# Kernel tuning notes

Measured on AMD Instinct MI355X. Metric: run time of the kernel, lower is better.

Reference implementation:

```python
import jax, jax.numpy as jnp
import numpy as np

B, N, NID, V, GH, PHI, RHO = 8, 256, 64, 128, 128, 256, 128
BN = B * N
EPS = 1e-5


def _layernorm(x, g, b):
    m = jnp.mean(x, axis=-1, keepdims=True)
    v = jnp.var(x, axis=-1, keepdims=True)
    return (x - m) * jax.lax.rsqrt(v + EPS) * g + b


def _edges(A):
    # dense adjacency -> flat batched edge list, exactly as mask.nonzero() ordering
    bidx = jnp.arange(B)[:, None, None]
    ii = jnp.arange(N)[None, :, None]
    jj = jnp.arange(N)[None, None, :]
    src = jnp.broadcast_to(bidx * N + ii, (B, N, N)).reshape(-1)  # edge_index[0] = b*N+i
    tgt = jnp.broadcast_to(bidx * N + jj, (B, N, N)).reshape(-1)  # edge_index[1] = b*N+j
    w = A.reshape(-1)
    valid = w != 0
    rel = (w > 0).astype(jnp.int32)
    return src, tgt, w, valid, rel


def _rgcn(H, src, tgt, valid, rel, Wrel, Wroot, bias):
    # torch_geometric RGCNConv: mean aggregation per relation at target + root + bias
    x_src = H[src]  # (E, d) gather
    out = H @ Wroot + bias
    for r in range(2):
        m = (valid & (rel == r)).astype(H.dtype)  # (E,)
        s = jax.ops.segment_sum(x_src * m[:, None], tgt, num_segments=BN)
        c = jax.ops.segment_sum(m, tgt, num_segments=BN)
        out = out + (s / jnp.maximum(c, 1.0)[:, None]) @ Wrel[r]
    return out


def setup_inputs() -> dict:
    key = jax.random.key(0)
    ks = jax.random.split(key, 24)
    p = lambda k, shape: jax.random.normal(k, shape, dtype=jnp.float32) * 0.02
    z = lambda *shape: jnp.zeros(shape, jnp.float32)
    return {
        "A": jax.random.normal(ks[0], (B, N, N), dtype=jnp.float32),
        "X": jax.random.normal(ks[1], (B, N, NID), dtype=jnp.float32),
        "home_mask": (jax.random.uniform(ks[2], (B, N)) > 0.5).astype(jnp.float32),
        "emb1_w": p(ks[3], (NID, V)), "emb1_b": z(V),
        "emb2_w": p(ks[4], (V, V)), "emb2_b": z(V),
        "rgcn_w_0": p(ks[5], (2, V, GH)), "rgcn_root_0": p(ks[6], (V, GH)), "rgcn_bias_0": z(GH),
        "lina_w_0": p(ks[7], (GH, GH)), "lina_b_0": z(GH),
        "linb_w_0": p(ks[8], (GH, GH)), "linb_b_0": z(GH),
        "rgcn_w_1": p(ks[9], (2, GH, GH)), "rgcn_root_1": p(ks[10], (GH, GH)), "rgcn_bias_1": z(GH),
        "lina_w_1": p(ks[11], (GH, GH)), "lina_b_1": z(GH),
        "linb_w_1": p(ks[12], (GH, GH)), "linb_b_1": z(GH),
        "norm_g": jnp.ones((GH,), jnp.float32), "norm_b": z(GH),
        "phi_w1": p(ks[13], (GH, PHI)), "phi_b1": z(PHI),
        "phi_w2": p(ks[14], (PHI, PHI)), "phi_b2": z(PHI),
        "rho_w1": p(ks[15], (PHI, RHO)), "rho_b1": z(RHO),
        "rho_w2": p(ks[16], (RHO, 1)), "rho_b2": z(1),
    }


def reference(A, X, home_mask, emb1_w, emb1_b, emb2_w, emb2_b,
              rgcn_w_0, rgcn_root_0, rgcn_bias_0, lina_w_0, lina_b_0, linb_w_0, linb_b_0,
              rgcn_w_1, rgcn_root_1, rgcn_bias_1, lina_w_1, lina_b_1, linb_w_1, linb_b_1,
              norm_g, norm_b, phi_w1, phi_b1, phi_w2, phi_b2,
              rho_w1, rho_b1, rho_w2, rho_b2):
    away_mask = 1.0 - home_mask
    H = jax.nn.relu(X @ emb1_w + emb1_b)
    H = (H @ emb2_w + emb2_b).reshape(BN, V)

    src, tgt, w, valid, rel = _edges(A)
    aw = jnp.abs(w) * valid.astype(w.dtype)  # |edge_weight|, zero for masked-out edges

    blocks = [
        (rgcn_w_0, rgcn_root_0, rgcn_bias_0, lina_w_0, lina_b_0, linb_w_0, linb_b_0),
        (rgcn_w_1, rgcn_root_1, rgcn_bias_1, lina_w_1, lina_b_1, linb_w_1, linb_b_1),
    ]
    agg = jnp.zeros_like(H)
    for (Wrel, Wroot, bias, law, lab, lbw, lbb) in blocks:
        H = H + agg
        H2 = _rgcn(H, src, tgt, valid, rel, Wrel, Wroot, bias)
        # gather-scale-scatter: agg[src] += H2[tgt] * |w|
        agg = jax.ops.segment_sum(H2[tgt] * aw[:, None], src, num_segments=BN)
        agg = jax.nn.relu(_layernorm(agg, norm_g, norm_b))  # dropout = identity (eval)
        agg = jax.nn.relu(agg @ law + lab)
        agg = agg @ lbw + lbb
    H = (H + agg).reshape(B, N, GH)

    # DeepSet phi (dropout = identity)
    h = jax.nn.relu(H @ phi_w1 + phi_b1)
    phi_out = jax.nn.relu(h @ phi_w2 + phi_b2)  # (B, N, PHI)

    home_sum = jnp.sum(phi_out * home_mask[:, :, None], axis=1)
    away_sum = jnp.sum(phi_out * away_mask[:, :, None], axis=1)

    def rho(s):
        return (jax.nn.relu(s @ rho_w1 + rho_b1) @ rho_w2 + rho_b2)[:, 0]

    out = rho(home_sum) - rho(away_sum)
    return 0.5 + 0.5 * jnp.tanh(out)  # (B,)
```

## Files before the change

kernel.cpp:

```cpp
#include <hip/hip_runtime.h>
#include <math.h>

#define NB 8

__global__ __launch_bounds__(512, 4) void k_embed(const float* __restrict__ X,
        const float* __restrict__ w1, const float* __restrict__ b1,
        const float* __restrict__ w2, const float* __restrict__ b2,
        float* __restrict__ H, float* __restrict__ pools) {
    const int r0 = blockIdx.x * 4;
    const int t = threadIdx.x, q = t & 31, u = t >> 5;
    __shared__ __align__(16) float part[8192];
    __shared__ __align__(16) float xq[256];
    __shared__ __align__(16) float h1q[512];
    if (blockIdx.x < 8) pools[blockIdx.x * 512 + t] = 0.f;
    if (t < 64) {
        float4 v;
        v.x = X[(size_t)(r0 + 0) * 64 + t];
        v.y = X[(size_t)(r0 + 1) * 64 + t];
        v.z = X[(size_t)(r0 + 2) * 64 + t];
        v.w = X[(size_t)(r0 + 3) * 64 + t];
        *(float4*)&xq[t * 4] = v;
    }
    __syncthreads();
    {
        float acc[16];
        #pragma unroll
        for (int i = 0; i < 16; ++i) acc[i] = 0.f;
        #pragma unroll
        for (int kk = 0; kk < 4; ++kk) {
            int k = u * 4 + kk;
            float4 w4 = *(const float4*)&w1[(size_t)k * 128 + q * 4];
            float wc[4] = {w4.x, w4.y, w4.z, w4.w};
            float4 x4 = *(const float4*)&xq[k * 4];
            float xr[4] = {x4.x, x4.y, x4.z, x4.w};
            #pragma unroll
            for (int r = 0; r < 4; ++r)
                #pragma unroll
                for (int c = 0; c < 4; ++c)
                    acc[r * 4 + c] = fmaf(xr[r], wc[c], acc[r * 4 + c]);
        }
        #pragma unroll
        for (int r = 0; r < 4; ++r)
            *(float4*)&part[u * 512 + r * 128 + q * 4] =
                make_float4(acc[r*4+0], acc[r*4+1], acc[r*4+2], acc[r*4+3]);
    }
    __syncthreads();
    {
        int r = t >> 7, f = t & 127;
        float s = b1[f];
        #pragma unroll
        for (int uu = 0; uu < 16; ++uu) s += part[uu * 512 + r * 128 + f];
        h1q[f * 4 + r] = fmaxf(s, 0.f);
    }
    __syncthreads();
    {
        float a2[16];
        #pragma unroll
        for (int i = 0; i < 16; ++i) a2[i] = 0.f;
        #pragma unroll
        for (int kk = 0; kk < 8; ++kk) {
            int k = u * 8 + kk;
            float4 w4 = *(const float4*)&w2[(size_t)k * 128 + q * 4];
            float wc[4] = {w4.x, w4.y, w4.z, w4.w};
            float4 h4 = *(const float4*)&h1q[k * 4];
            float hr[4] = {h4.x, h4.y, h4.z, h4.w};
            #pragma unroll
            for (int r = 0; r < 4; ++r)
                #pragma unroll
                for (int c = 0; c < 4; ++c)
                    a2[r * 4 + c] = fmaf(hr[r], wc[c], a2[r * 4 + c]);
        }
        #pragma unroll
        for (int r = 0; r < 4; ++r)
            *(float4*)&part[u * 512 + r * 128 + q * 4] =
                make_float4(a2[r*4+0], a2[r*4+1], a2[r*4+2], a2[r*4+3]);
    }
    __syncthreads();
    {
        int r = t >> 7, f = t & 127;
        float s = b2[f];
        #pragma unroll
        for (int uu = 0; uu < 16; ++uu) s += part[uu * 512 + r * 128 + f];
        H[(size_t)(r0 + r) * 128 + f] = s;
    }
}

__global__ __launch_bounds__(512, 4) void k_gcn1(
        const float* __restrict__ A, const float* __restrict__ H,
        const float* __restrict__ Wrel, const float* __restrict__ Wroot,
        const float* __restrict__ bias, float* __restrict__ H2) {
    const int b  = blockIdx.x >> 6;
    const int j0 = (blockIdx.x & 63) * 4;
    const int t = threadIdx.x, q = t & 31, u = t >> 5;
    __shared__ __align__(16) float maskM[2048];
    __shared__ __align__(16) float part[8192];
    __shared__ __align__(16) float pb[1536];
    __shared__ float cntp[256];
    __shared__ float cnt[8];
    const float* Ab = A + (size_t)b * 65536;
    const float* Hb = H + (size_t)b * 32768;
    const float* W0 = Wrel;
    const float* W1 = Wrel + 16384;

    if (t < 256) {
        float4 a = *(const float4*)(Ab + (size_t)t * 256 + j0);
        float4 m0, m1;
        m0.x = (a.x < 0.f) ? 1.f : 0.f; m1.x = (a.x > 0.f) ? 1.f : 0.f;
        m0.y = (a.y < 0.f) ? 1.f : 0.f; m1.y = (a.y > 0.f) ? 1.f : 0.f;
        m0.z = (a.z < 0.f) ? 1.f : 0.f; m1.z = (a.z > 0.f) ? 1.f : 0.f;
        m0.w = (a.w < 0.f) ? 1.f : 0.f; m1.w = (a.w > 0.f) ? 1.f : 0.f;
        *(float4*)&maskM[t * 8]     = m0;
        *(float4*)&maskM[t * 8 + 4] = m1;
    }
    __syncthreads();
    if (t < 256) {
        int chunk = t >> 3, slot = t & 7;
        float c = 0.f;
        #pragma unroll
        for (int qq = 0; qq < 8; ++qq) c += maskM[(chunk * 8 + qq) * 8 + slot];
        cntp[slot * 32 + chunk] = c;
    }
    float acc0[16], acc1[16];
    #pragma unroll
    for (int i = 0; i < 16; ++i) { acc0[i] = 0.f; acc1[i] = 0.f; }
    #pragma unroll 8
    for (int ii = 0; ii < 16; ++ii) {
        int i = u * 16 + ii;
        float4 h4 = *(const float4*)&Hb[(size_t)i * 128 + q * 4];
        float hc[4] = {h4.x, h4.y, h4.z, h4.w};
        float4 m0 = *(const float4*)&maskM[i * 8];
        float4 m1 = *(const float4*)&maskM[i * 8 + 4];
        float mr0[4] = {m0.x, m0.y, m0.z, m0.w};
        float mr1[4] = {m1.x, m1.y, m1.z, m1.w};
        #pragma unroll
        for (int r = 0; r < 4; ++r)
            #pragma unroll
            for (int c = 0; c < 4; ++c) {
                acc0[r * 4 + c] = fmaf(mr0[r], hc[c], acc0[r * 4 + c]);
                acc1[r * 4 + c] = fmaf(mr1[r], hc[c], acc1[r * 4 + c]);
            }
    }
    #pragma unroll
    for (int r = 0; r < 4; ++r)
        *(float4*)&part[u * 512 + r * 128 + q * 4] =
            make_float4(acc0[r*4+0], acc0[r*4+1], acc0[r*4+2], acc0[r*4+3]);
    if (t < 8) {
        float s = 0.f;
        #pragma unroll
        for (int c = 0; c < 32; ++c) s += cntp[t * 32 + c];
        cnt[t] = s;
    }
    __syncthreads();
    {
        int r = t >> 7, f = t & 127;
        float s = 0.f;
        #pragma unroll
        for (int uu = 0; uu < 16; ++uu) s += part[uu * 512 + r * 128 + f];
        pb[f * 12 + 4 + r] = s * (1.f / fmaxf(cnt[r], 1.f));
    }
    __syncthreads();
    #pragma unroll
    for (int r = 0; r < 4; ++r)
        *(float4*)&part[u * 512 + r * 128 + q * 4] =
            make_float4(acc1[r*4+0], acc1[r*4+1], acc1[r*4+2], acc1[r*4+3]);
    __syncthreads();
    {
        int r = t >> 7, f = t & 127;
        float s = 0.f;
        #pragma unroll
        for (int uu = 0; uu < 16; ++uu) s += part[uu * 512 + r * 128 + f];
        pb[f * 12 + 8 + r] = s * (1.f / fmaxf(cnt[4 + r], 1.f));
    }
    if (t < 128) {
        int r = t >> 5, fq = t & 31;
        float4 g4 = *(const float4*)(Hb + (size_t)(j0 + r) * 128 + fq * 4);
        pb[(fq * 4 + 0) * 12 + r] = g4.x;
        pb[(fq * 4 + 1) * 12 + r] = g4.y;
        pb[(fq * 4 + 2) * 12 + r] = g4.z;
        pb[(fq * 4 + 3) * 12 + r] = g4.w;
    }
    __syncthreads();
    float bcc[16];
    #pragma unroll
    for (int i = 0; i < 16; ++i) bcc[i] = 0.f;
    #pragma unroll 4
    for (int kk = 0; kk < 8; ++kk) {
        int k = u * 8 + kk;
        float4 wr = *(const float4*)&Wroot[(size_t)k * 128 + q * 4];
        float4 wa = *(const float4*)&W0[(size_t)k * 128 + q * 4];
        float4 wb = *(const float4*)&W1[(size_t)k * 128 + q * 4];
        float wrc[4] = {wr.x, wr.y, wr.z, wr.w};
        float wac[4] = {wa.x, wa.y, wa.z, wa.w};
        float wbc[4] = {wb.x, wb.y, wb.z, wb.w};
        float4 hv = *(const float4*)&pb[k * 12];
        float4 q0 = *(const float4*)&pb[k * 12 + 4];
        float4 q1 = *(const float4*)&pb[k * 12 + 8];
        float hr[4] = {hv.x, hv.y, hv.z, hv.w};
        float m0r[4] = {q0.x, q0.y, q0.z, q0.w};
        float m1r[4] = {q1.x, q1.y, q1.z, q1.w};
        #pragma unroll
        for (int r = 0; r < 4; ++r)
            #pragma unroll
            for (int c = 0; c < 4; ++c) {
                float v = bcc[r * 4 + c];
                v = fmaf(hr[r], wrc[c], v);
                v = fmaf(m0r[r], wac[c], v);
                v = fmaf(m1r[r], wbc[c], v);
                bcc[r * 4 + c] = v;
            }
    }
    #pragma unroll
    for (int r = 0; r < 4; ++r)
        *(float4*)&part[u * 512 + r * 128 + q * 4] =
            make_float4(bcc[r*4+0], bcc[r*4+1], bcc[r*4+2], bcc[r*4+3]);
    __syncthreads();
    {
        int r = t >> 7, f = t & 127;
        float s = bias[f];
        #pragma unroll
        for (int uu = 0; uu < 16; ++uu) s += part[uu * 512 + r * 128 + f];
        H2[(size_t)(b * 256 + j0 + r) * 128 + f] = s;
    }
}

__global__ __launch_bounds__(512, 4) void k_gcn2(
        const float* __restrict__ A, const float* __restrict__ H2,
        const float* __restrict__ g, const float* __restrict__ bta,
        const float* __restrict__ law, const float* __restrict__ lab,
        const float* __restrict__ lbw, const float* __restrict__ lbb,
        float* __restrict__ H) {
    const int b  = blockIdx.x >> 6;
    const int i0 = (blockIdx.x & 63) * 4;
    const int t = threadIdx.x, q = t & 31, u = t >> 5;
    __shared__ __align__(16) float part[8192];
    __shared__ __align__(16) float absA[1024];
    __shared__ __align__(16) float xq[512];
    __shared__ __align__(16) float uq[512];
    __shared__ float red[16];
    __shared__ float mi[8];
    const float* Ab  = A + (size_t)b * 65536;
    const float* H2b = H2 + (size_t)b * 32768;

    if (t < 256) {
        float4 av;
        av.x = fabsf(Ab[(size_t)(i0 + 0) * 256 + t]);
        av.y = fabsf(Ab[(size_t)(i0 + 1) * 256 + t]);
        av.z = fabsf(Ab[(size_t)(i0 + 2) * 256 + t]);
        av.w = fabsf(Ab[(size_t)(i0 + 3) * 256 + t]);
        *(float4*)&absA[t * 4] = av;
    }
    __syncthreads();
    float acc[16];
    #pragma unroll
    for (int i = 0; i < 16; ++i) acc[i] = 0.f;
    #pragma unroll 8
    for (int jj = 0; jj < 16; ++jj) {
        int j = u * 16 + jj;
        float4 h4 = *(const float4*)&H2b[(size_t)j * 128 + q * 4];
        float hc[4] = {h4.x, h4.y, h4.z, h4.w};
        float4 a4 = *(const float4*)&absA[j * 4];
        float ar[4] = {a4.x, a4.y, a4.z, a4.w};
        #pragma unroll
        for (int r = 0; r < 4; ++r)
            #pragma unroll
            for (int c = 0; c < 4; ++c)
                acc[r * 4 + c] = fmaf(ar[r], hc[c], acc[r * 4 + c]);
    }
    #pragma unroll
    for (int r = 0; r < 4; ++r)
        *(float4*)&part[u * 512 + r * 128 + q * 4] =
            make_float4(acc[r*4+0], acc[r*4+1], acc[r*4+2], acc[r*4+3]);
    __syncthreads();
    const int rr = t >> 7, ff = t & 127;
    float x;
    {
        float s = 0.f;
        #pragma unroll
        for (int uu = 0; uu < 16; ++uu) s += part[uu * 512 + rr * 128 + ff];
        x = s;
        float s2 = x * x;
        float sw = x;
        #pragma unroll
        for (int o = 32; o > 0; o >>= 1) {
            sw += __shfl_down(sw, o, 64);
            s2 += __shfl_down(s2, o, 64);
        }
        int w = (t >> 6) & 1;
        if ((t & 63) == 0) {
            red[(rr * 2 + w) * 2]     = sw;
            red[(rr * 2 + w) * 2 + 1] = s2;
        }
    }
    __syncthreads();
    if (t < 4) {
        float s  = red[t * 4]     + red[t * 4 + 2];
        float s2 = red[t * 4 + 1] + red[t * 4 + 3];
        float m = s * (1.f / 128.f);
        float v = s2 * (1.f / 128.f) - m * m;
        mi[t * 2] = m;
        mi[t * 2 + 1] = rsqrtf(v + 1e-5f);
    }
    __syncthreads();
    xq[ff * 4 + rr] = fmaxf((x - mi[rr * 2]) * mi[rr * 2 + 1] * g[ff] + bta[ff], 0.f);
    __syncthreads();
    float u1[16];
    #pragma unroll
    for (int i = 0; i < 16; ++i) u1[i] = 0.f;
    #pragma unroll
    for (int kk = 0; kk < 8; ++kk) {
        int k = u * 8 + kk;
        float4 w4 = *(const float4*)&law[(size_t)k * 128 + q * 4];
        float wc[4] = {w4.x, w4.y, w4.z, w4.w};
        float4 x4 = *(const float4*)&xq[k * 4];
        float xr[4] = {x4.x, x4.y, x4.z, x4.w};
        #pragma unroll
        for (int r = 0; r < 4; ++r)
            #pragma unroll
            for (int c = 0; c < 4; ++c)
                u1[r * 4 + c] = fmaf(xr[r], wc[c], u1[r * 4 + c]);
    }
    #pragma unroll
    for (int r = 0; r < 4; ++r)
        *(float4*)&part[u * 512 + r * 128 + q * 4] =
            make_float4(u1[r*4+0], u1[r*4+1], u1[r*4+2], u1[r*4+3]);
    __syncthreads();
    {
        float s = lab[ff];
        #pragma unroll
        for (int uu = 0; uu < 16; ++uu) s += part[uu * 512 + rr * 128 + ff];
        uq[ff * 4 + rr] = fmaxf(s, 0.f);
    }
    __syncthreads();
    float u2[16];
    #pragma unroll
    for (int i = 0; i < 16; ++i) u2[i] = 0.f;
    #pragma unroll
    for (int kk = 0; kk < 8; ++kk) {
        int k = u * 8 + kk;
        float4 w4 = *(const float4*)&lbw[(size_t)k * 128 + q * 4];
        float wc[4] = {w4.x, w4.y, w4.z, w4.w};
        float4 x4 = *(const float4*)&uq[k * 4];
        float xr[4] = {x4.x, x4.y, x4.z, x4.w};
        #pragma unroll
        for (int r = 0; r < 4; ++r)
            #pragma unroll
            for (int c = 0; c < 4; ++c)
                u2[r * 4 + c] = fmaf(xr[r], wc[c], u2[r * 4 + c]);
    }
    #pragma unroll
    for (int r = 0; r < 4; ++r)
        *(float4*)&part[u * 512 + r * 128 + q * 4] =
            make_float4(u2[r*4+0], u2[r*4+1], u2[r*4+2], u2[r*4+3]);
    __syncthreads();
    {
        float s = lbb[ff];
        #pragma unroll
        for (int uu = 0; uu < 16; ++uu) s += part[uu * 512 + rr * 128 + ff];
        size_t idx = (size_t)(b * 256 + i0 + rr) * 128 + ff;
        H[idx] = s + H[idx];
    }
}

__global__ __launch_bounds__(512, 4) void k_deepset(
        const float* __restrict__ H, const float* __restrict__ hm,
        const float* __restrict__ w1, const float* __restrict__ b1,
        const float* __restrict__ w2, const float* __restrict__ b2,
        float* __restrict__ hsum, float* __restrict__ asum) {
    const int r0 = blockIdx.x * 4;
    const int b  = blockIdx.x >> 6;
    const int t  = threadIdx.x, q = t & 63, u = t >> 6;
    __shared__ __align__(16) float part[8192];
    __shared__ __align__(16) float ph2[1024];
    __shared__ __align__(16) float hraw[512];
    __shared__ float hmv[4];
    if (t < 128) {
        float4 g4 = *(const float4*)&H[(size_t)r0 * 128 + t * 4];
        *(float4*)&hraw[t * 4] = g4;
    }
    if (t < 4) hmv[t] = hm[r0 + t];
    __syncthreads();
    float acc[16];
    #pragma unroll
    for (int i = 0; i < 16; ++i) acc[i] = 0.f;
    #pragma unroll 8
    for (int kk = 0; kk < 16; ++kk) {
        int k = u * 16 + kk;
        float4 w4 = *(const float4*)&w1[(size_t)k * 256 + q * 4];
        float wc[4] = {w4.x, w4.y, w4.z, w4.w};
        float hr[4];
        #pragma unroll
        for (int r = 0; r < 4; ++r) hr[r] = hraw[r * 128 + k];
        #pragma unroll
        for (int r = 0; r < 4; ++r)
            #pragma unroll
            for (int c = 0; c < 4; ++c)
                acc[r * 4 + c] = fmaf(hr[r], wc[c], acc[r * 4 + c]);
    }
    #pragma unroll
    for (int r = 0; r < 4; ++r)
        *(float4*)&part[u * 1024 + r * 256 + q * 4] =
            make_float4(acc[r*4+0], acc[r*4+1], acc[r*4+2], acc[r*4+3]);
    __syncthreads();
    {
        #pragma unroll
        for (int e = 0; e < 2; ++e) {
            int idx = e * 512 + t;
            int r = idx >> 8, f = idx & 255;
            float s = b1[f];
            #pragma unroll
            for (int uu = 0; uu < 8; ++uu) s += part[uu * 1024 + r * 256 + f];
            ph2[r * 256 + f] = fmaxf(s, 0.f);
        }
    }
    __syncthreads();
    float a2[16];
    #pragma unroll
    for (int i = 0; i < 16; ++i) a2[i] = 0.f;
    #pragma unroll 8
    for (int kk = 0; kk < 32; ++kk) {
        int k = u * 32 + kk;
        float4 w4 = *(const float4*)&w2[(size_t)k * 256 + q * 4];
        float wc[4] = {w4.x, w4.y, w4.z, w4.w};
        float pr[4];
        #pragma unroll
        for (int r = 0; r < 4; ++r) pr[r] = ph2[r * 256 + k];
        #pragma unroll
        for (int r = 0; r < 4; ++r)
            #pragma unroll
            for (int c = 0; c < 4; ++c)
                a2[r * 4 + c] = fmaf(pr[r], wc[c], a2[r * 4 + c]);
    }
    #pragma unroll
    for (int r = 0; r < 4; ++r)
        *(float4*)&part[u * 1024 + r * 256 + q * 4] =
            make_float4(a2[r*4+0], a2[r*4+1], a2[r*4+2], a2[r*4+3]);
    __syncthreads();
    if (t < 256) {
        float bb = b2[t];
        float hp = 0.f, sp = 0.f;
        #pragma unroll
        for (int r = 0; r < 4; ++r) {
            float s = bb;
            #pragma unroll
            for (int uu = 0; uu < 8; ++uu) s += part[uu * 1024 + r * 256 + t];
            float p = fmaxf(s, 0.f);
            sp += p;
            hp = fmaf(p, hmv[r], hp);
        }
        atomicAdd(&hsum[b * 256 + t], hp);
        atomicAdd(&asum[b * 256 + t], sp - hp);
    }
}

__global__ __launch_bounds__(256) void k_rho(const float* __restrict__ hsum,
        const float* __restrict__ asum,
        const float* __restrict__ w1, const float* __restrict__ b1,
        const float* __restrict__ w2, const float* __restrict__ b2,
        float* __restrict__ out) {
    const int bIdx = blockIdx.x;
    const int t = threadIdx.x, q = t & 31, u = t >> 5;
    __shared__ __align__(16) float part[2048];
    __shared__ __align__(16) float sv[512];
    __shared__ float wsv[2];
    sv[t] = hsum[bIdx * 256 + t];
    sv[256 + t] = asum[bIdx * 256 + t];
    __syncthreads();
    float aH[4] = {0.f, 0.f, 0.f, 0.f}, aA[4] = {0.f, 0.f, 0.f, 0.f};
    #pragma unroll 8
    for (int kk = 0; kk < 32; ++kk) {
        int k = u * 32 + kk;
        float4 w4 = *(const float4*)&w1[(size_t)k * 128 + q * 4];
        float sh = sv[k], sa = sv[256 + k];
        aH[0] = fmaf(sh, w4.x, aH[0]); aA[0] = fmaf(sa, w4.x, aA[0]);
        aH[1] = fmaf(sh, w4.y, aH[1]); aA[1] = fmaf(sa, w4.y, aA[1]);
        aH[2] = fmaf(sh, w4.z, aH[2]); aA[2] = fmaf(sa, w4.z, aA[2]);
        aH[3] = fmaf(sh, w4.w, aH[3]); aA[3] = fmaf(sa, w4.w, aA[3]);
    }
    *(float4*)&part[u * 256 + q * 4]       = make_float4(aH[0], aH[1], aH[2], aH[3]);
    *(float4*)&part[u * 256 + 128 + q * 4] = make_float4(aA[0], aA[1], aA[2], aA[3]);
    __syncthreads();
    if (t < 64) {
        int vec = t >> 5, fq = t & 31;
        float4 s = make_float4(0.f, 0.f, 0.f, 0.f);
        #pragma unroll
        for (int uu = 0; uu < 8; ++uu) {
            float4 p = *(const float4*)&part[uu * 256 + vec * 128 + fq * 4];
            s.x += p.x; s.y += p.y; s.z += p.z; s.w += p.w;
        }
        float4 bb = *(const float4*)&b1[fq * 4];
        float4 w2q = *(const float4*)&w2[fq * 4];
        float p = fmaxf(s.x + bb.x, 0.f) * w2q.x
                + fmaxf(s.y + bb.y, 0.f) * w2q.y
                + fmaxf(s.z + bb.z, 0.f) * w2q.z
                + fmaxf(s.w + bb.w, 0.f) * w2q.w;
        #pragma unroll
        for (int o = 16; o > 0; o >>= 1) p += __shfl_down(p, o, 32);
        if ((t & 31) == 0) wsv[vec] = p;
    }
    __syncthreads();
    if (t == 0) out[bIdx] = 0.5f + 0.5f * tanhf(wsv[0] - wsv[1]);
}

extern "C" void kernel_launch(void* const* d_in, const int* in_sizes, int n_in,
                              void* d_out, int out_size, void* d_ws, size_t ws_size,
                              hipStream_t stream) {
    const float* A         = (const float*)d_in[0];
    const float* X         = (const float*)d_in[1];
    const float* home_mask = (const float*)d_in[2];
    const float* emb1_w    = (const float*)d_in[3];
    const float* emb1_b    = (const float*)d_in[4];
    const float* emb2_w    = (const float*)d_in[5];
    const float* emb2_b    = (const float*)d_in[6];
    const float* rgcn_w[2]    = { (const float*)d_in[7],  (const float*)d_in[14] };
    const float* rgcn_root[2] = { (const float*)d_in[8],  (const float*)d_in[15] };
    const float* rgcn_bias[2] = { (const float*)d_in[9],  (const float*)d_in[16] };
    const float* lina_w[2]    = { (const float*)d_in[10], (const float*)d_in[17] };
    const float* lina_b[2]    = { (const float*)d_in[11], (const float*)d_in[18] };
    const float* linb_w[2]    = { (const float*)d_in[12], (const float*)d_in[19] };
    const float* linb_b[2]    = { (const float*)d_in[13], (const float*)d_in[20] };
    const float* norm_g  = (const float*)d_in[21];
    const float* norm_b  = (const float*)d_in[22];
    const float* phi_w1  = (const float*)d_in[23];
    const float* phi_b1  = (const float*)d_in[24];
    const float* phi_w2  = (const float*)d_in[25];
    const float* phi_b2  = (const float*)d_in[26];
    const float* rho_w1  = (const float*)d_in[27];
    const float* rho_b1  = (const float*)d_in[28];
    const float* rho_w2  = (const float*)d_in[29];
    const float* rho_b2  = (const float*)d_in[30];
    float* out = (float*)d_out;

    float* ws   = (float*)d_ws;
    float* H    = ws;
    float* H2   = ws + 262144;
    float* hsum = ws + 524288;
    float* asum = ws + 526336;

    k_embed<<<512, 512, 0, stream>>>(X, emb1_w, emb1_b, emb2_w, emb2_b, H, hsum);

    for (int it = 0; it < 2; ++it) {
        k_gcn1<<<512, 512, 0, stream>>>(A, H, rgcn_w[it], rgcn_root[it],
                                        rgcn_bias[it], H2);
        k_gcn2<<<512, 512, 0, stream>>>(A, H2, norm_g, norm_b,
                                        lina_w[it], lina_b[it],
                                        linb_w[it], linb_b[it], H);
    }

    k_deepset<<<512, 512, 0, stream>>>(H, home_mask, phi_w1, phi_b1,
                                       phi_w2, phi_b2, hsum, asum);
    k_rho<<<NB, 256, 0, stream>>>(hsum, asum, rho_w1, rho_b1, rho_w2, rho_b2, out);
}
```

Measured before the change: 189.3 us.

## Split DeepSet phi into two tiled GEMM kernels with 64-row tiles

Replaces the single fused DeepSet kernel, which processed 4 rows per block and re-read the full phi weight matrices for every block, with two kernels. Each new kernel tiles 64 rows by 32 columns, so each weight element is fetched far fewer times. The intermediate activation goes through a global buffer, and the home/away pooling now uses a wavefront shuffle reduction before the atomics. The cost is an extra launch, a global round trip for the 2048x256 intermediate, and lower per-thread register reuse.

```diff
diff --git a/kernel.cpp b/kernel.cpp
--- a/kernel.cpp
+++ b/kernel.cpp
@@ -361,94 +361,99 @@
     }
 }
 
-__global__ __launch_bounds__(512, 4) void k_deepset(
-        const float* __restrict__ H, const float* __restrict__ hm,
-        const float* __restrict__ w1, const float* __restrict__ b1,
+__global__ __launch_bounds__(512, 2) void k_phi1(
+        const float* __restrict__ H, const float* __restrict__ w1,
+        const float* __restrict__ b1, float* __restrict__ PH1) {
+    const int rt = blockIdx.x >> 3, ct = blockIdx.x & 7;
+    const int r0 = rt * 64, c0 = ct * 32;
+    const int t = threadIdx.x;
+    __shared__ __align__(16) float Hl[64 * 132];
+    #pragma unroll
+    for (int e = 0; e < 4; ++e) {
+        int idx = e * 512 + t;
+        int rr = idx >> 5, k4 = idx & 31;
+        float4 v = *(const float4*)&H[(size_t)(r0 + rr) * 128 + k4 * 4];
+        *(float4*)&Hl[rr * 132 + k4 * 4] = v;
+    }
+    __syncthreads();
+    const int rr = t >> 3, cq = t & 7;
+    float a0 = 0.f, a1 = 0.f, a2 = 0.f, a3 = 0.f;
+    #pragma unroll 8
+    for (int k = 0; k < 128; ++k) {
+        float4 w4 = *(const float4*)&w1[(size_t)k * 256 + c0 + cq * 4];
+        float x = Hl[rr * 132 + k];
+        a0 = fmaf(x, w4.x, a0);
+        a1 = fmaf(x, w4.y, a1);
+        a2 = fmaf(x, w4.z, a2);
+        a3 = fmaf(x, w4.w, a3);
+    }
+    float4 bb = *(const float4*)&b1[c0 + cq * 4];
+    float4 o = make_float4(fmaxf(a0 + bb.x, 0.f), fmaxf(a1 + bb.y, 0.f),
+                           fmaxf(a2 + bb.z, 0.f), fmaxf(a3 + bb.w, 0.f));
+    *(float4*)&PH1[(size_t)(r0 + rr) * 256 + c0 + cq * 4] = o;
+}
+
+__global__ __launch_bounds__(512, 2) void k_phi2(
+        const float* __restrict__ PH1, const float* __restrict__ hm,
         const float* __restrict__ w2, const float* __restrict__ b2,
         float* __restrict__ hsum, float* __restrict__ asum) {
-    const int r0 = blockIdx.x * 4;
-    const int b  = blockIdx.x >> 6;
-    const int t  = threadIdx.x, q = t & 63, u = t >> 6;
-    __shared__ __align__(16) float part[8192];
-    __shared__ __align__(16) float ph2[1024];
-    __shared__ __align__(16) float hraw[512];
-    __shared__ float hmv[4];
-    if (t < 128) {
-        float4 g4 = *(const float4*)&H[(size_t)r0 * 128 + t * 4];
-        *(float4*)&hraw[t * 4] = g4;
-    }
-    if (t < 4) hmv[t] = hm[r0 + t];
-    __syncthreads();
-    float acc[16];
-    #pragma unroll
-    for (int i = 0; i < 16; ++i) acc[i] = 0.f;
+    const int rt = blockIdx.x >> 3, ct = blockIdx.x & 7;
+    const int r0 = rt * 64, c0 = ct * 32;
+    const int b = r0 >> 8;
+    const int t = threadIdx.x;
+    __shared__ __align__(16) float Pl[64 * 260];
+    __shared__ float redH[8][32];
+    __shared__ float redS[8][32];
+    __shared__ float hmv[64];
+    #pragma unroll
+    for (int e = 0; e < 8; ++e) {
+        int idx = e * 512 + t;
+        int rr = idx >> 6, k4 = idx & 63;
+        float4 v = *(const float4*)&PH1[(size_t)(r0 + rr) * 256 + k4 * 4];
+        *(float4*)&Pl[rr * 260 + k4 * 4] = v;
+    }
+    if (t < 64) hmv[t] = hm[r0 + t];
+    __syncthreads();
+    const int rr = t >> 3, cq = t & 7;
+    float a0 = 0.f, a1 = 0.f, a2 = 0.f, a3 = 0.f;
     #pragma unroll 8
-    for (int kk = 0; kk < 16; ++kk) {
-        int k = u * 16 + kk;
-        float4 w4 = *(const float4*)&w1[(size_t)k * 256 + q * 4];
-        float wc[4] = {w4.x, w4.y, w4.z, w4.w};
-        float hr[4];
-        #pragma unroll
-        for (int r = 0; r < 4; ++r) hr[r] = hraw[r * 128 + k];
-        #pragma unroll
-        for (int r = 0; r < 4; ++r)
-            #pragma unroll
-            for (int c = 0; c < 4; ++c)
-                acc[r * 4 + c] = fmaf(hr[r], wc[c], acc[r * 4 + c]);
-    }
-    #pragma unroll
-    for (int r = 0; r < 4; ++r)
-        *(float4*)&part[u * 1024 + r * 256 + q * 4] =
-            make_float4(acc[r*4+0], acc[r*4+1], acc[r*4+2], acc[r*4+3]);
-    __syncthreads();
-    {
-        #pragma unroll
-        for (int e = 0; e < 2; ++e) {
-            int idx = e * 512 + t;
-            int r = idx >> 8, f = idx & 255;
-            float s = b1[f];
-            #pragma unroll
-            for (int uu = 0; uu < 8; ++uu) s += part[uu * 1024 + r * 256 + f];
-            ph2[r * 256 + f] = fmaxf(s, 0.f);
-        }
-    }
-    __syncthreads();
-    float a2[16];
-    #pragma unroll
-    for (int i = 0; i < 16; ++i) a2[i] = 0.f;
-    #pragma unroll 8
-    for (int kk = 0; kk < 32; ++kk) {
-        int k = u * 32 + kk;
-        float4 w4 = *(const float4*)&w2[(size_t)k * 256 + q * 4];
-        float wc[4] = {w4.x, w4.y, w4.z, w4.w};
-        float pr[4];
-        #pragma unroll
-        for (int r = 0; r < 4; ++r) pr[r] = ph2[r * 256 + k];
-        #pragma unroll
-        for (int r = 0; r < 4; ++r)
-            #pragma unroll
-            for (int c = 0; c < 4; ++c)
-                a2[r * 4 + c] = fmaf(pr[r], wc[c], a2[r * 4 + c]);
-    }
-    #pragma unroll
-    for (int r = 0; r < 4; ++r)
-        *(float4*)&part[u * 1024 + r * 256 + q * 4] =
-            make_float4(a2[r*4+0], a2[r*4+1], a2[r*4+2], a2[r*4+3]);
-    __syncthreads();
-    if (t < 256) {
-        float bb = b2[t];
-        float hp = 0.f, sp = 0.f;
-        #pragma unroll
-        for (int r = 0; r < 4; ++r) {
-            float s = bb;
-            #pragma unroll
-            for (int uu = 0; uu < 8; ++uu) s += part[uu * 1024 + r * 256 + t];
-            float p = fmaxf(s, 0.f);
-            sp += p;
-            hp = fmaf(p, hmv[r], hp);
-        }
-        atomicAdd(&hsum[b * 256 + t], hp);
-        atomicAdd(&asum[b * 256 + t], sp - hp);
+    for (int k = 0; k < 256; ++k) {
+        float4 w4 = *(const float4*)&w2[(size_t)k * 256 + c0 + cq * 4];
+        float x = Pl[rr * 260 + k];
+        a0 = fmaf(x, w4.x, a0);
+        a1 = fmaf(x, w4.y, a1);
+        a2 = fmaf(x, w4.z, a2);
+        a3 = fmaf(x, w4.w, a3);
+    }
+    float4 bb = *(const float4*)&b2[c0 + cq * 4];
+    float p0 = fmaxf(a0 + bb.x, 0.f), p1 = fmaxf(a1 + bb.y, 0.f);
+    float p2 = fmaxf(a2 + bb.z, 0.f), p3 = fmaxf(a3 + bb.w, 0.f);
+    float hmr = hmv[rr];
+    float hp[4] = {p0 * hmr, p1 * hmr, p2 * hmr, p3 * hmr};
+    float sp[4] = {p0, p1, p2, p3};
+    #pragma unroll
+    for (int j = 0; j < 4; ++j) {
+        #pragma unroll
+        for (int o = 32; o >= 8; o >>= 1) {
+            hp[j] += __shfl_down(hp[j], o, 64);
+            sp[j] += __shfl_down(sp[j], o, 64);
+        }
+    }
+    if ((t & 63) < 8) {
+        int wv = t >> 6;
+        #pragma unroll
+        for (int j = 0; j < 4; ++j) {
+            redH[wv][cq * 4 + j] = hp[j];
+            redS[wv][cq * 4 + j] = sp[j];
+        }
+    }
+    __syncthreads();
+    if (t < 32) {
+        float sh = 0.f, sa = 0.f;
+        #pragma unroll
+        for (int wv = 0; wv < 8; ++wv) { sh += redH[wv][t]; sa += redS[wv][t]; }
+        atomicAdd(&hsum[b * 256 + c0 + t], sh);
+        atomicAdd(&asum[b * 256 + c0 + t], sa - sh);
     }
 }
 
@@ -535,6 +540,7 @@
     float* H2   = ws + 262144;
     float* hsum = ws + 524288;
     float* asum = ws + 526336;
+    float* PH1  = ws + 528384;
 
     k_embed<<<512, 512, 0, stream>>>(X, emb1_w, emb1_b, emb2_w, emb2_b, H, hsum);
 
@@ -546,7 +552,7 @@
                                         linb_w[it], linb_b[it], H);
     }
 
-    k_deepset<<<512, 512, 0, stream>>>(H, home_mask, phi_w1, phi_b1,
-                                       phi_w2, phi_b2, hsum, asum);
+    k_phi1<<<256, 512, 0, stream>>>(H, phi_w1, phi_b1, PH1);
+    k_phi2<<<256, 512, 0, stream>>>(PH1, home_mask, phi_w2, phi_b2, hsum, asum);
     k_rho<<<NB, 256, 0, stream>>>(hsum, asum, rho_w1, rho_b1, rho_w2, rho_b2, out);
 }
```

New measurement: 201.7 us. +6.5%, slower.
